# Kernel optimization log

Hardware: AMD Instinct MI355X
Metric: run time of the kernel (lower is better)

The kernel has to match this reference:

```python
import jax, jax.numpy as jnp
import numpy as np

B, L, C, N, K = 8, 4096, 256, 512, 15


def setup_inputs() -> dict:
    key = jax.random.key(0)
    k0, k1, k2, k3 = jax.random.split(key, 4)
    x = jax.random.normal(k0, (B, L, C), dtype=jnp.float32)
    m = min(C, N)
    w_in_w = jax.random.normal(k1, (N, C), dtype=jnp.float32) * 0.01
    w_in_w = w_in_w.at[:m, :m].add(jnp.eye(m, dtype=jnp.float32))
    w_in_b = jnp.zeros((N,), dtype=jnp.float32)
    W = jax.random.normal(k2, (N, N), dtype=jnp.float32) * 0.01
    b = jnp.zeros((N,), dtype=jnp.float32)
    w_out_w = jax.random.normal(k3, (C, N), dtype=jnp.float32) * 0.01
    w_out_w = w_out_w.at[:m, :m].add(jnp.eye(m, dtype=jnp.float32))
    w_out_b = jnp.zeros((C,), dtype=jnp.float32)
    return {"x": x, "w_in_w": w_in_w, "w_in_b": w_in_b, "W": W, "b": b,
            "w_out_w": w_out_w, "w_out_b": w_out_b}


def reference(x, w_in_w, w_in_b, W, b, w_out_w, w_out_b):
    Bn, Ln, Cn = x.shape
    xf = x.reshape(Bn * Ln, Cn)                      # (BL, C)
    c = xf @ w_in_w.T + w_in_b                       # (BL, N)
    Ws = 0.5 * (W + W.T)                             # symmetrize=True
    a0 = jnp.zeros_like(c)

    def step(a, _):
        # F.linear(a, Ws, b) == a @ Ws.T + b
        a = jnp.tanh(a @ Ws.T + b + c)
        return a, None

    a, _ = jax.lax.scan(step, a0, None, length=K)
    y = (a @ w_out_w.T + w_out_b).reshape(Bn, Ln, Cn)
    return (y, x - y)
```

## Files before the change

kernel.cpp:

```cpp
#include <hip/hip_runtime.h>
#include <hip/hip_bf16.h>
#include <stdint.h>

#define THREADS 512

typedef __bf16 bf16x8 __attribute__((ext_vector_type(8)));
typedef float f32x4 __attribute__((ext_vector_type(4)));

#define WS_WS_OFF    0
#define WS_WINH_OFF  (512*512*2)
#define WS_WINL_OFF  (WS_WINH_OFF + 512*256*2)
#define WS_WOUTH_OFF (WS_WINL_OFF + 512*256*2)
#define WS_WOUTL_OFF (WS_WOUTH_OFF + 256*512*2)
#define WS_CVEC_OFF  (WS_WOUTL_OFF + 256*512*2)

__device__ __forceinline__ unsigned short f2bf(float f) {
  union { float f; unsigned int u; } v; v.f = f;
  unsigned int r = (v.u + 0x7fffu + ((v.u >> 16) & 1u)) >> 16;
  return (unsigned short)r;
}
__device__ __forceinline__ float bf2f(unsigned short h) {
  union { unsigned int u; float f; } v; v.u = ((unsigned int)h) << 16;
  return v.f;
}

__device__ __forceinline__ void gload16(const void* g, void* l) {
  __builtin_amdgcn_global_load_lds(
      (const __attribute__((address_space(1))) unsigned int*)g,
      (__attribute__((address_space(3))) unsigned int*)l,
      16, 0, 0);
}

__global__ void prep_kernel(const float* __restrict__ W,
                            const float* __restrict__ w_in_w,
                            const float* __restrict__ w_out_w,
                            const float* __restrict__ w_in_b,
                            const float* __restrict__ bvec,
                            unsigned char* __restrict__ ws) {
  int i = blockIdx.x * blockDim.x + threadIdx.x;
  unsigned short* Wsb   = (unsigned short*)(ws + WS_WS_OFF);
  unsigned short* WinH  = (unsigned short*)(ws + WS_WINH_OFF);
  unsigned short* WinL  = (unsigned short*)(ws + WS_WINL_OFF);
  unsigned short* WoutH = (unsigned short*)(ws + WS_WOUTH_OFF);
  unsigned short* WoutL = (unsigned short*)(ws + WS_WOUTL_OFF);
  float* cvec = (float*)(ws + WS_CVEC_OFF);
  if (i < 512*512) {
    int r = i >> 9, c = i & 511;
    Wsb[i] = f2bf(0.5f * (W[i] + W[c*512 + r]));
  } else if (i < 512*512 + 512*256) {
    int j = i - 512*512;
    float w = w_in_w[j];
    unsigned short h = f2bf(w);
    WinH[j] = h;
    WinL[j] = f2bf(w - bf2f(h));
  } else if (i < 512*512 + 512*256 + 256*512) {
    int j = i - 512*512 - 512*256;
    float w = w_out_w[j];
    unsigned short h = f2bf(w);
    WoutH[j] = h;
    WoutL[j] = f2bf(w - bf2f(h));
  } else if (i < 512*512 + 512*256 + 256*512 + 512) {
    int j = i - 512*512 - 512*256 - 256*512;
    cvec[j] = w_in_b[j] + bvec[j];
  }
}

__global__ void __launch_bounds__(THREADS, 2)
attractor_kernel(const float* __restrict__ x,
                 const unsigned char* __restrict__ ws,
                 const float* __restrict__ w_out_b,
                 float* __restrict__ out) {
  __shared__ unsigned char smem[131072];
  unsigned char* Albase = smem;
  unsigned char* Axh    = smem;
  unsigned char* Axl    = smem + 32768;
  unsigned char* Tbuf0  = smem + 65536;
  unsigned char* Tbuf1  = smem + 98304;

  const int tid  = threadIdx.x;
  const int lane = tid & 63;
  const int l15  = lane & 15;
  const int l4   = lane >> 4;
  const int wave = tid >> 6;
  const int wm   = wave >> 2;
  const int wn   = wave & 3;
  const int m0   = blockIdx.x * 64;

  const unsigned char* gWs    = ws + WS_WS_OFF;
  const unsigned char* gWinH  = ws + WS_WINH_OFF;
  const unsigned char* gWinL  = ws + WS_WINL_OFF;
  const unsigned char* gWoutH = ws + WS_WOUTH_OFF;
  const unsigned char* gWoutL = ws + WS_WOUTL_OFF;
  const float* cvec = (const float*)(ws + WS_CVEC_OFF);

  {
    const float4* xt = (const float4*)(x + (size_t)m0 * 256);
#pragma unroll
    for (int p = 0; p < 8; ++p) {
      int i = tid + p * THREADS;
      float4 v = xt[i];
      int m  = i >> 6;
      int bc = (i & 63) * 8;
      unsigned short hx = f2bf(v.x), hy = f2bf(v.y), hz = f2bf(v.z), hw = f2bf(v.w);
      unsigned short lx = f2bf(v.x - bf2f(hx)), ly = f2bf(v.y - bf2f(hy));
      unsigned short lz = f2bf(v.z - bf2f(hz)), lw = f2bf(v.w - bf2f(hw));
      *(uint2*)(Axh + m * 512 + bc) =
          make_uint2((unsigned int)hx | ((unsigned int)hy << 16),
                     (unsigned int)hz | ((unsigned int)hw << 16));
      *(uint2*)(Axl + m * 512 + bc) =
          make_uint2((unsigned int)lx | ((unsigned int)ly << 16),
                     (unsigned int)lz | ((unsigned int)lw << 16));
    }
  }

  f32x4 acc[2][8];
#pragma unroll
  for (int nf = 0; nf < 8; ++nf) {
    float cv = cvec[wn * 128 + nf * 16 + l15];
    f32x4 v = {cv, cv, cv, cv};
    acc[0][nf] = v;
    acc[1][nf] = v;
  }

#pragma unroll 1
  for (int ks = 0; ks < 8; ++ks) {
    __syncthreads();
    for (int c = tid; c < 2048; c += THREADS) {
      int d = c << 4; int row = d >> 6; int col = d & 63;
      size_t g = (size_t)row * 512 + (size_t)ks * 64 + col;
      gload16(gWinH + g, Tbuf0 + d);
      gload16(gWinL + g, Tbuf1 + d);
    }
    __syncthreads();
    int akb = ks * 64 + l4 * 16;
    bf16x8 xh0 = *(const bf16x8*)(Axh + (wm*32      + l15) * 512 + akb);
    bf16x8 xh1 = *(const bf16x8*)(Axh + (wm*32 + 16 + l15) * 512 + akb);
    bf16x8 xl0 = *(const bf16x8*)(Axl + (wm*32      + l15) * 512 + akb);
    bf16x8 xl1 = *(const bf16x8*)(Axl + (wm*32 + 16 + l15) * 512 + akb);
#pragma unroll
    for (int nf = 0; nf < 8; ++nf) {
      int bp = (wn*128 + nf*16 + l15) * 64 + l4 * 16;
      bf16x8 bh = *(const bf16x8*)(Tbuf0 + bp);
      bf16x8 bl = *(const bf16x8*)(Tbuf1 + bp);
      acc[0][nf] = __builtin_amdgcn_mfma_f32_16x16x32_bf16(xh0, bh, acc[0][nf], 0, 0, 0);
      acc[0][nf] = __builtin_amdgcn_mfma_f32_16x16x32_bf16(xh0, bl, acc[0][nf], 0, 0, 0);
      acc[0][nf] = __builtin_amdgcn_mfma_f32_16x16x32_bf16(xl0, bh, acc[0][nf], 0, 0, 0);
      acc[1][nf] = __builtin_amdgcn_mfma_f32_16x16x32_bf16(xh1, bh, acc[1][nf], 0, 0, 0);
      acc[1][nf] = __builtin_amdgcn_mfma_f32_16x16x32_bf16(xh1, bl, acc[1][nf], 0, 0, 0);
      acc[1][nf] = __builtin_amdgcn_mfma_f32_16x16x32_bf16(xl1, bh, acc[1][nf], 0, 0, 0);
    }
  }
  __syncthreads();

  f32x4 cfrag[2][8];
#pragma unroll
  for (int mf = 0; mf < 2; ++mf)
#pragma unroll
    for (int nf = 0; nf < 8; ++nf)
      cfrag[mf][nf] = acc[mf][nf];

  auto write_a = [&]() {
#pragma unroll
    for (int mf = 0; mf < 2; ++mf) {
#pragma unroll
      for (int nf = 0; nf < 8; ++nf) {
        int n2 = (wn*128 + nf*16 + l15) * 2;
#pragma unroll
        for (int r = 0; r < 4; ++r) {
          int m = wm*32 + mf*16 + l4*4 + r;
          float t  = __expf(2.0f * acc[mf][nf][r]);
          float th = 1.0f - __fdividef(2.0f, t + 1.0f);
          *(unsigned short*)(Albase + m*1024 + n2) = f2bf(th);
        }
      }
    }
  };
  write_a();

  auto stageW = [&](unsigned char* lds, const unsigned char* g0) {
    for (int c = tid; c < 2048; c += THREADS) {
      int d = c << 4;
      gload16(g0 + (size_t)(d >> 6) * 1024 + (d & 63), lds + d);
    }
  };
#pragma unroll 1
  for (int it = 0; it < 14; ++it) {
    stageW(Tbuf0, gWs);
#pragma unroll
    for (int mf = 0; mf < 2; ++mf)
#pragma unroll
      for (int nf = 0; nf < 8; ++nf)
        acc[mf][nf] = cfrag[mf][nf];
#pragma unroll 1
    for (int ks = 0; ks < 16; ++ks) {
      __syncthreads();
      unsigned char* curb = (ks & 1) ? Tbuf1 : Tbuf0;
      if (ks < 15) stageW((ks & 1) ? Tbuf0 : Tbuf1, gWs + (ks + 1) * 64);
      int akb = ks * 64 + l4 * 16;
      bf16x8 a0 = *(const bf16x8*)(Albase + (wm*32      + l15) * 1024 + akb);
      bf16x8 a1 = *(const bf16x8*)(Albase + (wm*32 + 16 + l15) * 1024 + akb);
#pragma unroll
      for (int nf = 0; nf < 8; ++nf) {
        bf16x8 bb = *(const bf16x8*)(curb + (wn*128 + nf*16 + l15) * 64 + l4 * 16);
        acc[0][nf] = __builtin_amdgcn_mfma_f32_16x16x32_bf16(a0, bb, acc[0][nf], 0, 0, 0);
        acc[1][nf] = __builtin_amdgcn_mfma_f32_16x16x32_bf16(a1, bb, acc[1][nf], 0, 0, 0);
      }
    }
    __syncthreads();
    write_a();
  }

  f32x4 oacc[2][4];
#pragma unroll
  for (int nf = 0; nf < 4; ++nf) {
    float wob = w_out_b[wn*64 + nf*16 + l15];
    f32x4 v = {wob, wob, wob, wob};
    oacc[0][nf] = v;
    oacc[1][nf] = v;
  }
  auto stageOut = [&](int ks, unsigned char* buf) {
    for (int c = tid; c < 1024; c += THREADS) {
      int d = c << 4; int row = d >> 6; int col = d & 63;
      size_t g = (size_t)row * 1024 + (size_t)ks * 64 + col;
      gload16(gWoutH + g, buf + d);
      gload16(gWoutL + g, buf + 16384 + d);
    }
  };
  stageOut(0, Tbuf0);
#pragma unroll 1
  for (int ks = 0; ks < 16; ++ks) {
    __syncthreads();
    unsigned char* cur = (ks & 1) ? Tbuf1 : Tbuf0;
    if (ks < 15) stageOut(ks + 1, (ks & 1) ? Tbuf0 : Tbuf1);
    int akb = ks * 64 + l4 * 16;
    bf16x8 a0 = *(const bf16x8*)(Albase + (wm*32      + l15) * 1024 + akb);
    bf16x8 a1 = *(const bf16x8*)(Albase + (wm*32 + 16 + l15) * 1024 + akb);
#pragma unroll
    for (int nf = 0; nf < 4; ++nf) {
      int bp = (wn*64 + nf*16 + l15) * 64 + l4 * 16;
      bf16x8 bh = *(const bf16x8*)(cur + bp);
      bf16x8 bl = *(const bf16x8*)(cur + 16384 + bp);
      oacc[0][nf] = __builtin_amdgcn_mfma_f32_16x16x32_bf16(a0, bh, oacc[0][nf], 0, 0, 0);
      oacc[0][nf] = __builtin_amdgcn_mfma_f32_16x16x32_bf16(a0, bl, oacc[0][nf], 0, 0, 0);
      oacc[1][nf] = __builtin_amdgcn_mfma_f32_16x16x32_bf16(a1, bh, oacc[1][nf], 0, 0, 0);
      oacc[1][nf] = __builtin_amdgcn_mfma_f32_16x16x32_bf16(a1, bl, oacc[1][nf], 0, 0, 0);
    }
  }

  const size_t HALF = (size_t)8 * 4096 * 256;
#pragma unroll
  for (int mf = 0; mf < 2; ++mf) {
#pragma unroll
    for (int nf = 0; nf < 4; ++nf) {
      int j = wn*64 + nf*16 + l15;
#pragma unroll
      for (int r = 0; r < 4; ++r) {
        int m = m0 + wm*32 + mf*16 + l4*4 + r;
        size_t idx = (size_t)m * 256 + j;
        float y = oacc[mf][nf][r];
        out[idx]        = y;
        out[HALF + idx] = x[idx] - y;
      }
    }
  }
}

extern "C" void kernel_launch(void* const* d_in, const int* in_sizes, int n_in,
                              void* d_out, int out_size, void* d_ws, size_t ws_size,
                              hipStream_t stream) {
  const float* x       = (const float*)d_in[0];
  const float* w_in_w  = (const float*)d_in[1];
  const float* w_in_b  = (const float*)d_in[2];
  const float* W       = (const float*)d_in[3];
  const float* b       = (const float*)d_in[4];
  const float* w_out_w = (const float*)d_in[5];
  const float* w_out_b = (const float*)d_in[6];
  float* out = (float*)d_out;
  unsigned char* ws = (unsigned char*)d_ws;

  int total = 512*512 + 512*256 + 256*512 + 512;
  prep_kernel<<<(total + 255) / 256, 256, 0, stream>>>(W, w_in_w, w_out_w, w_in_b, b, ws);
  attractor_kernel<<<512, THREADS, 0, stream>>>(x, ws, w_out_b, out);
}
```

Before: 666.6 us.

## Register-staged double-buffered weight loads with XOR-swizzled LDS layout

```diff
diff --git a/kernel.cpp b/kernel.cpp
--- a/kernel.cpp
+++ b/kernel.cpp
@@ -22,13 +22,6 @@
 __device__ __forceinline__ float bf2f(unsigned short h) {
   union { unsigned int u; float f; } v; v.u = ((unsigned int)h) << 16;
   return v.f;
-}
-
-__device__ __forceinline__ void gload16(const void* g, void* l) {
-  __builtin_amdgcn_global_load_lds(
-      (const __attribute__((address_space(1))) unsigned int*)g,
-      (__attribute__((address_space(3))) unsigned int*)l,
-      16, 0, 0);
 }
 
 __global__ void prep_kernel(const float* __restrict__ W,
@@ -93,6 +86,15 @@
   const unsigned char* gWoutL = ws + WS_WOUTL_OFF;
   const float* cvec = (const float*)(ws + WS_CVEC_OFF);
 
+  const int srow  = tid >> 2;
+  const int scol  = (tid & 3) * 16;
+  const int swcol = scol ^ (((srow >> 1) & 3) << 4);
+  const int stile = srow * 64 + swcol;
+  const int bswz  = (l4 * 16) ^ (((l15 >> 1) & 3) << 4);
+  const int aswz  = (l15 & 7) << 4;
+  const int arow0 = (wm * 32 + l15) * 1024;
+  const int arow1 = arow0 + 16 * 1024;
+
   {
     const float4* xt = (const float4*)(x + (size_t)m0 * 256);
 #pragma unroll
@@ -104,12 +106,11 @@
       unsigned short hx = f2bf(v.x), hy = f2bf(v.y), hz = f2bf(v.z), hw = f2bf(v.w);
       unsigned short lx = f2bf(v.x - bf2f(hx)), ly = f2bf(v.y - bf2f(hy));
       unsigned short lz = f2bf(v.z - bf2f(hz)), lw = f2bf(v.w - bf2f(hw));
-      *(uint2*)(Axh + m * 512 + bc) =
-          make_uint2((unsigned int)hx | ((unsigned int)hy << 16),
-                     (unsigned int)hz | ((unsigned int)hw << 16));
-      *(uint2*)(Axl + m * 512 + bc) =
-          make_uint2((unsigned int)lx | ((unsigned int)ly << 16),
-                     (unsigned int)lz | ((unsigned int)lw << 16));
+      int off = m * 512 + (bc ^ ((m & 7) << 4));
+      *(uint2*)(Axh + off) = make_uint2((unsigned int)hx | ((unsigned int)hy << 16),
+                                        (unsigned int)hz | ((unsigned int)hw << 16));
+      *(uint2*)(Axl + off) = make_uint2((unsigned int)lx | ((unsigned int)ly << 16),
+                                        (unsigned int)lz | ((unsigned int)lw << 16));
     }
   }
 
@@ -122,32 +123,48 @@
     acc[1][nf] = v;
   }
 
+  {
+    const unsigned char* gH = gWinH + (size_t)srow * 512 + scol;
+    const unsigned char* gL = gWinL + (size_t)srow * 512 + scol;
+    uint4 rH[4], rL[4];
+#pragma unroll
+    for (int k = 0; k < 4; ++k) {
+      rH[k] = *(const uint4*)(gH + k * 65536);
+      rL[k] = *(const uint4*)(gL + k * 65536);
+    }
 #pragma unroll 1
-  for (int ks = 0; ks < 8; ++ks) {
-    __syncthreads();
-    for (int c = tid; c < 2048; c += THREADS) {
-      int d = c << 4; int row = d >> 6; int col = d & 63;
-      size_t g = (size_t)row * 512 + (size_t)ks * 64 + col;
-      gload16(gWinH + g, Tbuf0 + d);
-      gload16(gWinL + g, Tbuf1 + d);
-    }
-    __syncthreads();
-    int akb = ks * 64 + l4 * 16;
-    bf16x8 xh0 = *(const bf16x8*)(Axh + (wm*32      + l15) * 512 + akb);
-    bf16x8 xh1 = *(const bf16x8*)(Axh + (wm*32 + 16 + l15) * 512 + akb);
-    bf16x8 xl0 = *(const bf16x8*)(Axl + (wm*32      + l15) * 512 + akb);
-    bf16x8 xl1 = *(const bf16x8*)(Axl + (wm*32 + 16 + l15) * 512 + akb);
-#pragma unroll
-    for (int nf = 0; nf < 8; ++nf) {
-      int bp = (wn*128 + nf*16 + l15) * 64 + l4 * 16;
-      bf16x8 bh = *(const bf16x8*)(Tbuf0 + bp);
-      bf16x8 bl = *(const bf16x8*)(Tbuf1 + bp);
-      acc[0][nf] = __builtin_amdgcn_mfma_f32_16x16x32_bf16(xh0, bh, acc[0][nf], 0, 0, 0);
-      acc[0][nf] = __builtin_amdgcn_mfma_f32_16x16x32_bf16(xh0, bl, acc[0][nf], 0, 0, 0);
-      acc[0][nf] = __builtin_amdgcn_mfma_f32_16x16x32_bf16(xl0, bh, acc[0][nf], 0, 0, 0);
-      acc[1][nf] = __builtin_amdgcn_mfma_f32_16x16x32_bf16(xh1, bh, acc[1][nf], 0, 0, 0);
-      acc[1][nf] = __builtin_amdgcn_mfma_f32_16x16x32_bf16(xh1, bl, acc[1][nf], 0, 0, 0);
-      acc[1][nf] = __builtin_amdgcn_mfma_f32_16x16x32_bf16(xl1, bh, acc[1][nf], 0, 0, 0);
+    for (int ks = 0; ks < 8; ++ks) {
+      __syncthreads();
+#pragma unroll
+      for (int k = 0; k < 4; ++k) {
+        *(uint4*)(Tbuf0 + stile + k * 8192) = rH[k];
+        *(uint4*)(Tbuf1 + stile + k * 8192) = rL[k];
+      }
+      if (ks < 7) {
+#pragma unroll
+        for (int k = 0; k < 4; ++k) {
+          rH[k] = *(const uint4*)(gH + (ks + 1) * 64 + k * 65536);
+          rL[k] = *(const uint4*)(gL + (ks + 1) * 64 + k * 65536);
+        }
+      }
+      __syncthreads();
+      int akb = ks * 64 + l4 * 16;
+      bf16x8 xh0 = *(const bf16x8*)(Axh + (wm*32      + l15) * 512 + (akb ^ aswz));
+      bf16x8 xh1 = *(const bf16x8*)(Axh + (wm*32 + 16 + l15) * 512 + (akb ^ aswz));
+      bf16x8 xl0 = *(const bf16x8*)(Axl + (wm*32      + l15) * 512 + (akb ^ aswz));
+      bf16x8 xl1 = *(const bf16x8*)(Axl + (wm*32 + 16 + l15) * 512 + (akb ^ aswz));
+#pragma unroll
+      for (int nf = 0; nf < 8; ++nf) {
+        int bp = (wn*128 + nf*16 + l15) * 64 + bswz;
+        bf16x8 bh = *(const bf16x8*)(Tbuf0 + bp);
+        bf16x8 bl = *(const bf16x8*)(Tbuf1 + bp);
+        acc[0][nf] = __builtin_amdgcn_mfma_f32_16x16x32_bf16(xh0, bh, acc[0][nf], 0, 0, 0);
+        acc[0][nf] = __builtin_amdgcn_mfma_f32_16x16x32_bf16(xh0, bl, acc[0][nf], 0, 0, 0);
+        acc[0][nf] = __builtin_amdgcn_mfma_f32_16x16x32_bf16(xl0, bh, acc[0][nf], 0, 0, 0);
+        acc[1][nf] = __builtin_amdgcn_mfma_f32_16x16x32_bf16(xh1, bh, acc[1][nf], 0, 0, 0);
+        acc[1][nf] = __builtin_amdgcn_mfma_f32_16x16x32_bf16(xh1, bl, acc[1][nf], 0, 0, 0);
+        acc[1][nf] = __builtin_amdgcn_mfma_f32_16x16x32_bf16(xl1, bh, acc[1][nf], 0, 0, 0);
+      }
     }
   }
   __syncthreads();
@@ -170,43 +187,78 @@
           int m = wm*32 + mf*16 + l4*4 + r;
           float t  = __expf(2.0f * acc[mf][nf][r]);
           float th = 1.0f - __fdividef(2.0f, t + 1.0f);
-          *(unsigned short*)(Albase + m*1024 + n2) = f2bf(th);
+          *(unsigned short*)(Albase + m*1024 + (n2 ^ ((m & 7) << 4))) = f2bf(th);
         }
       }
     }
   };
+
+  const unsigned char* gWsT = gWs + (size_t)srow * 1024 + scol;
+  uint4 rA[4], rB[4];
+#pragma unroll
+  for (int k = 0; k < 4; ++k) rA[k] = *(const uint4*)(gWsT + 0*64 + k * 131072);
+#pragma unroll
+  for (int k = 0; k < 4; ++k) rB[k] = *(const uint4*)(gWsT + 1*64 + k * 131072);
   write_a();
 
-  auto stageW = [&](unsigned char* lds, const unsigned char* g0) {
-    for (int c = tid; c < 2048; c += THREADS) {
-      int d = c << 4;
-      gload16(g0 + (size_t)(d >> 6) * 1024 + (d & 63), lds + d);
-    }
-  };
+  uint4 rHA[2], rLA[2], rHB[2], rLB[2];
+  const unsigned char* gOH = gWoutH + (size_t)srow * 1024 + scol;
+  const unsigned char* gOL = gWoutL + (size_t)srow * 1024 + scol;
+
+#define RSTEP(KS, CUR, NXT, RNOW, RNXT)                                         \
+  {                                                                             \
+    if ((KS) + 2 <= 15) {                                                       \
+      _Pragma("unroll")                                                         \
+      for (int k = 0; k < 4; ++k)                                               \
+        RNOW[k] = *(const uint4*)(gWsT + ((KS) + 2) * 64 + k * 131072);         \
+    }                                                                           \
+    int akb = (KS) * 64 + l4 * 16;                                              \
+    bf16x8 a0 = *(const bf16x8*)(Albase + arow0 + (akb ^ aswz));                \
+    bf16x8 a1 = *(const bf16x8*)(Albase + arow1 + (akb ^ aswz));                \
+    _Pragma("unroll")                                                           \
+    for (int nf = 0; nf < 8; ++nf) {                                            \
+      bf16x8 bb = *(const bf16x8*)((CUR) + (wn*128 + nf*16 + l15) * 64 + bswz); \
+      acc[0][nf] = __builtin_amdgcn_mfma_f32_16x16x32_bf16(a0, bb, acc[0][nf], 0, 0, 0); \
+      acc[1][nf] = __builtin_amdgcn_mfma_f32_16x16x32_bf16(a1, bb, acc[1][nf], 0, 0, 0); \
+    }                                                                           \
+    if ((KS) < 15) {                                                            \
+      _Pragma("unroll")                                                         \
+      for (int k = 0; k < 4; ++k)                                               \
+        *(uint4*)((NXT) + stile + k * 8192) = RNXT[k];                          \
+    }                                                                           \
+    __syncthreads();                                                            \
+  }
+
 #pragma unroll 1
   for (int it = 0; it < 14; ++it) {
-    stageW(Tbuf0, gWs);
+    __syncthreads();
+#pragma unroll
+    for (int k = 0; k < 4; ++k) *(uint4*)(Tbuf0 + stile + k * 8192) = rA[k];
 #pragma unroll
     for (int mf = 0; mf < 2; ++mf)
 #pragma unroll
       for (int nf = 0; nf < 8; ++nf)
         acc[mf][nf] = cfrag[mf][nf];
+    __syncthreads();
 #pragma unroll 1
-    for (int ks = 0; ks < 16; ++ks) {
-      __syncthreads();
-      unsigned char* curb = (ks & 1) ? Tbuf1 : Tbuf0;
-      if (ks < 15) stageW((ks & 1) ? Tbuf0 : Tbuf1, gWs + (ks + 1) * 64);
-      int akb = ks * 64 + l4 * 16;
-      bf16x8 a0 = *(const bf16x8*)(Albase + (wm*32      + l15) * 1024 + akb);
-      bf16x8 a1 = *(const bf16x8*)(Albase + (wm*32 + 16 + l15) * 1024 + akb);
-#pragma unroll
-      for (int nf = 0; nf < 8; ++nf) {
-        bf16x8 bb = *(const bf16x8*)(curb + (wn*128 + nf*16 + l15) * 64 + l4 * 16);
-        acc[0][nf] = __builtin_amdgcn_mfma_f32_16x16x32_bf16(a0, bb, acc[0][nf], 0, 0, 0);
-        acc[1][nf] = __builtin_amdgcn_mfma_f32_16x16x32_bf16(a1, bb, acc[1][nf], 0, 0, 0);
-      }
-    }
-    __syncthreads();
+    for (int ks = 0; ks < 16; ks += 2) {
+      RSTEP(ks,     Tbuf0, Tbuf1, rA, rB);
+      RSTEP(ks + 1, Tbuf1, Tbuf0, rB, rA);
+    }
+    if (it < 13) {
+#pragma unroll
+      for (int k = 0; k < 4; ++k) rA[k] = *(const uint4*)(gWsT + 0*64 + k * 131072);
+#pragma unroll
+      for (int k = 0; k < 4; ++k) rB[k] = *(const uint4*)(gWsT + 1*64 + k * 131072);
+    } else {
+#pragma unroll
+      for (int k = 0; k < 2; ++k) {
+        rHA[k] = *(const uint4*)(gOH + 0*64 + k * 131072);
+        rLA[k] = *(const uint4*)(gOL + 0*64 + k * 131072);
+        rHB[k] = *(const uint4*)(gOH + 1*64 + k * 131072);
+        rLB[k] = *(const uint4*)(gOL + 1*64 + k * 131072);
+      }
+    }
     write_a();
   }
 
@@ -218,33 +270,50 @@
     oacc[0][nf] = v;
     oacc[1][nf] = v;
   }
-  auto stageOut = [&](int ks, unsigned char* buf) {
-    for (int c = tid; c < 1024; c += THREADS) {
-      int d = c << 4; int row = d >> 6; int col = d & 63;
-      size_t g = (size_t)row * 1024 + (size_t)ks * 64 + col;
-      gload16(gWoutH + g, buf + d);
-      gload16(gWoutL + g, buf + 16384 + d);
-    }
-  };
-  stageOut(0, Tbuf0);
+
+#define CSTEP(KS, CUR, NXT, RHN, RLN, RHX, RLX)                                 \
+  {                                                                             \
+    if ((KS) + 2 <= 15) {                                                       \
+      _Pragma("unroll")                                                         \
+      for (int k = 0; k < 2; ++k) {                                             \
+        RHN[k] = *(const uint4*)(gOH + ((KS) + 2) * 64 + k * 131072);           \
+        RLN[k] = *(const uint4*)(gOL + ((KS) + 2) * 64 + k * 131072);           \
+      }                                                                         \
+    }                                                                           \
+    int akb = (KS) * 64 + l4 * 16;                                              \
+    bf16x8 a0 = *(const bf16x8*)(Albase + arow0 + (akb ^ aswz));                \
+    bf16x8 a1 = *(const bf16x8*)(Albase + arow1 + (akb ^ aswz));                \
+    _Pragma("unroll")                                                           \
+    for (int nf = 0; nf < 4; ++nf) {                                            \
+      int bp = (wn*64 + nf*16 + l15) * 64 + bswz;                               \
+      bf16x8 bh = *(const bf16x8*)((CUR) + bp);                                 \
+      bf16x8 bl = *(const bf16x8*)((CUR) + 16384 + bp);                         \
+      oacc[0][nf] = __builtin_amdgcn_mfma_f32_16x16x32_bf16(a0, bh, oacc[0][nf], 0, 0, 0); \
+      oacc[0][nf] = __builtin_amdgcn_mfma_f32_16x16x32_bf16(a0, bl, oacc[0][nf], 0, 0, 0); \
+      oacc[1][nf] = __builtin_amdgcn_mfma_f32_16x16x32_bf16(a1, bh, oacc[1][nf], 0, 0, 0); \
+      oacc[1][nf] = __builtin_amdgcn_mfma_f32_16x16x32_bf16(a1, bl, oacc[1][nf], 0, 0, 0); \
+    }                                                                           \
+    if ((KS) < 15) {                                                            \
+      _Pragma("unroll")                                                         \
+      for (int k = 0; k < 2; ++k) {                                             \
+        *(uint4*)((NXT) + stile + k * 8192) = RHX[k];                           \
+        *(uint4*)((NXT) + 16384 + stile + k * 8192) = RLX[k];                   \
+      }                                                                         \
+    }                                                                           \
+    __syncthreads();                                                            \
+  }
+
+  __syncthreads();
+#pragma unroll
+  for (int k = 0; k < 2; ++k) {
+    *(uint4*)(Tbuf0 + stile + k * 8192) = rHA[k];
+    *(uint4*)(Tbuf0 + 16384 + stile + k * 8192) = rLA[k];
+  }
+  __syncthreads();
 #pragma unroll 1
-  for (int ks = 0; ks < 16; ++ks) {
-    __syncthreads();
-    unsigned char* cur = (ks & 1) ? Tbuf1 : Tbuf0;
-    if (ks < 15) stageOut(ks + 1, (ks & 1) ? Tbuf0 : Tbuf1);
-    int akb = ks * 64 + l4 * 16;
-    bf16x8 a0 = *(const bf16x8*)(Albase + (wm*32      + l15) * 1024 + akb);
-    bf16x8 a1 = *(const bf16x8*)(Albase + (wm*32 + 16 + l15) * 1024 + akb);
-#pragma unroll
-    for (int nf = 0; nf < 4; ++nf) {
-      int bp = (wn*64 + nf*16 + l15) * 64 + l4 * 16;
-      bf16x8 bh = *(const bf16x8*)(cur + bp);
-      bf16x8 bl = *(const bf16x8*)(cur + 16384 + bp);
-      oacc[0][nf] = __builtin_amdgcn_mfma_f32_16x16x32_bf16(a0, bh, oacc[0][nf], 0, 0, 0);
-      oacc[0][nf] = __builtin_amdgcn_mfma_f32_16x16x32_bf16(a0, bl, oacc[0][nf], 0, 0, 0);
-      oacc[1][nf] = __builtin_amdgcn_mfma_f32_16x16x32_bf16(a1, bh, oacc[1][nf], 0, 0, 0);
-      oacc[1][nf] = __builtin_amdgcn_mfma_f32_16x16x32_bf16(a1, bl, oacc[1][nf], 0, 0, 0);
-    }
+  for (int ks = 0; ks < 16; ks += 2) {
+    CSTEP(ks,     Tbuf0, Tbuf1, rHA, rLA, rHB, rLB);
+    CSTEP(ks + 1, Tbuf1, Tbuf0, rHB, rLB, rHA, rLA);
   }
 
   const size_t HALF = (size_t)8 * 4096 * 256;
```

New measurement: 1.222 ms. 1.83x slower.
